# Performance work log

Hardware: AMD Instinct MI355X
Metric: run time of the kernel (lower is better)

The kernel has to match this reference:

```python
import jax, jax.numpy as jnp
import numpy as np

N, E, G, D, L, EA = 100000, 1600000, 128, 128, 3, 7
BN_EPS = 1e-5


def _bn(x, g, b, m, v):
    # eval-mode BatchNorm1d with running stats
    return (x - m) * (g / jnp.sqrt(v + BN_EPS)) + b


def setup_inputs() -> dict:
    key = jax.random.key(0)
    ks = iter(jax.random.split(key, 64))
    nrm = lambda shape, s: jax.random.normal(next(ks), shape, jnp.float32) * s
    unif = lambda shape: jax.random.uniform(next(ks), shape, jnp.float32) * 0.5 + 0.5
    inp = {
        # forward tensor args
        'x': jnp.zeros((N,), jnp.int32),  # indices into Embedding(1, D) -> all zero
        'edge_index': jax.random.randint(next(ks), (2, E), 0, N, jnp.int32),
        'edge_attr': nrm((E, EA), 1.0),
        'batch': jnp.sort(jax.random.randint(next(ks), (N,), 0, G, jnp.int32)),
        # embeddings
        'node_emb': nrm((1, D), 1.0),
        'vn_emb': nrm((1, D), 0.1),
        # per-layer GINConv params (stacked on leading layer dim)
        'edge_W': nrm((L, EA, D), EA ** -0.5), 'edge_b': jnp.zeros((L, D), jnp.float32),
        'eps': jnp.zeros((L,), jnp.float32),
        'mlp_W1': nrm((L, D, 2 * D), D ** -0.5), 'mlp_b1': jnp.zeros((L, 2 * D), jnp.float32),
        'mbn_g': jnp.ones((L, 2 * D), jnp.float32), 'mbn_b': jnp.zeros((L, 2 * D), jnp.float32),
        'mbn_m': nrm((L, 2 * D), 0.1), 'mbn_v': unif((L, 2 * D)),
        'mlp_W2': nrm((L, 2 * D, D), (2 * D) ** -0.5), 'mlp_b2': jnp.zeros((L, D), jnp.float32),
        # outer per-layer BatchNorm
        'bn_g': jnp.ones((L, D), jnp.float32), 'bn_b': jnp.zeros((L, D), jnp.float32),
        'bn_m': nrm((L, D), 0.1), 'bn_v': unif((L, D)),
        # virtual-node MLPs (L-1 of them)
        'vn_W1': nrm((L - 1, D, 2 * D), D ** -0.5), 'vn_b1': jnp.zeros((L - 1, 2 * D), jnp.float32),
        'vbn1_g': jnp.ones((L - 1, 2 * D), jnp.float32), 'vbn1_b': jnp.zeros((L - 1, 2 * D), jnp.float32),
        'vbn1_m': nrm((L - 1, 2 * D), 0.1), 'vbn1_v': unif((L - 1, 2 * D)),
        'vn_W2': nrm((L - 1, 2 * D, D), (2 * D) ** -0.5), 'vn_b2': jnp.zeros((L - 1, D), jnp.float32),
        'vbn2_g': jnp.ones((L - 1, D), jnp.float32), 'vbn2_b': jnp.zeros((L - 1, D), jnp.float32),
        'vbn2_m': nrm((L - 1, D), 0.1), 'vbn2_v': unif((L - 1, D)),
    }
    return inp


def reference(x, edge_index, edge_attr, batch, node_emb, vn_emb,
              edge_W, edge_b, eps, mlp_W1, mlp_b1, mbn_g, mbn_b, mbn_m, mbn_v,
              mlp_W2, mlp_b2, bn_g, bn_b, bn_m, bn_v,
              vn_W1, vn_b1, vbn1_g, vbn1_b, vbn1_m, vbn1_v,
              vn_W2, vn_b2, vbn2_g, vbn2_b, vbn2_m, vbn2_v):
    src, dst = edge_index[0], edge_index[1]
    h = node_emb[x]                                # [N, D] node encoder gather
    vn = jnp.broadcast_to(vn_emb[0], (G, D))       # virtual node per graph
    for l in range(L):
        h_in = h + vn[batch]                       # broadcast virtual node to nodes
        # GINConv
        e = edge_attr @ edge_W[l] + edge_b[l]      # [E, D]
        msg = jax.nn.relu(h_in[src] + e)           # gather + edge fuse
        agg = jax.ops.segment_sum(msg, dst, num_segments=N)
        z = (1.0 + eps[l]) * h_in + agg
        z = jax.nn.relu(_bn(z @ mlp_W1[l] + mlp_b1[l], mbn_g[l], mbn_b[l], mbn_m[l], mbn_v[l]))
        h2 = z @ mlp_W2[l] + mlp_b2[l]
        # outer BatchNorm (+ relu except last layer; dropout is identity in eval)
        h2 = _bn(h2, bn_g[l], bn_b[l], bn_m[l], bn_v[l])
        h = h2 if l == L - 1 else jax.nn.relu(h2)
        if l < L - 1:
            vt = jax.ops.segment_sum(h_in, batch, num_segments=G) + vn  # global_add_pool
            t = jax.nn.relu(_bn(vt @ vn_W1[l] + vn_b1[l], vbn1_g[l], vbn1_b[l], vbn1_m[l], vbn1_v[l]))
            vn = jax.nn.relu(_bn(t @ vn_W2[l] + vn_b2[l], vbn2_g[l], vbn2_b[l], vbn2_m[l], vbn2_v[l]))
    return h  # JK == 'last'
```

## Files before the change

kernel.cpp:

```cpp
#include <hip/hip_runtime.h>
#include <hip/hip_bf16.h>

#define NN 100000
#define NP 100032
#define EE 1600000
#define GG 128
#define DD 128
#define LL 3
#define EAA 7
#define BN_EPS 1e-5f

typedef __attribute__((ext_vector_type(8))) short bf16x8;
typedef __attribute__((ext_vector_type(4))) float f32x4;
typedef __attribute__((ext_vector_type(4))) unsigned short u16x4;
typedef _Float16 f16x2 __attribute__((ext_vector_type(2)));

__device__ __forceinline__ unsigned short f2bf(float x) {
    unsigned int u = __float_as_uint(x);
    u = (u + 0x7FFF + ((u >> 16) & 1)) >> 16;
    return (unsigned short)u;
}
__device__ __forceinline__ float bf2f(unsigned short h) {
    return __uint_as_float(((unsigned int)h) << 16);
}
__device__ __forceinline__ float bflo(unsigned int u) {
    return __uint_as_float(u << 16);
}
__device__ __forceinline__ float bfhi(unsigned int u) {
    return __uint_as_float(u & 0xFFFF0000u);
}
__device__ __forceinline__ unsigned int pkf16(float a, float b) {
    f16x2 v = {(_Float16)a, (_Float16)b};
    return __builtin_bit_cast(unsigned int, v);
}

#if __has_builtin(__builtin_amdgcn_fdot2)
#define DOT2(q, w, c) __builtin_amdgcn_fdot2((q), (w), (c), false)
#else
__device__ __forceinline__ float dot2_sw(f16x2 a, f16x2 b, float c) {
    return fmaf((float)a.x, (float)b.x, fmaf((float)a.y, (float)b.y, c));
}
#define DOT2(q, w, c) dot2_sw((q), (w), (c))
#endif

__global__ __launch_bounds__(256) void init_kernel(
    const int* __restrict__ x, const float* __restrict__ node_emb,
    const float* __restrict__ vn_emb, float* __restrict__ h,
    float* __restrict__ vn)
{
    long i = (long)blockIdx.x * 256 + threadIdx.x;
    if (i < (long)NN * DD) {
        int node = (int)(i >> 7), d = (int)(i & 127);
        h[i] = node_emb[(long)x[node] * DD + d];
    }
    if (i < GG * DD) vn[i] = vn_emb[i & 127];
}

#define R1 8
__global__ __launch_bounds__(256) void hin_kernel(
    float* __restrict__ hbuf,
    unsigned short* __restrict__ h16,
    const float* __restrict__ vn,
    const int* __restrict__ batch,
    const float* __restrict__ eps,
    float* __restrict__ agg,
    float* __restrict__ vt,
    int layer, int accum_vt, int write_agg)
{
    const int d  = threadIdx.x & 127;
    const int rg = threadIdx.x >> 7;
    const float epl = 1.0f + eps[layer];
    const long row0 = (long)blockIdx.x * (R1 * 2);

    float vacc = 0.0f;
    int   vb   = -1;
    #pragma unroll
    for (int r = 0; r < R1; ++r) {
        long row = row0 + rg + 2 * r;
        if (row >= NN) break;
        int b = batch[row];
        long idx = row * DD + d;
        float hv = hbuf[idx] + vn[(long)b * DD + d];
        hbuf[idx] = hv;
        h16[idx]  = f2bf(hv);
        if (write_agg) agg[idx] = epl * hv;
        if (accum_vt) {
            if (b != vb) {
                if (vb >= 0) atomicAdd(&vt[(long)vb * DD + d], vacc);
                vb = b; vacc = 0.0f;
            }
            vacc += hv;
        }
    }
    if (accum_vt && vb >= 0) atomicAdd(&vt[(long)vb * DD + d], vacc);
}

__global__ __launch_bounds__(256) void vt_kernel(
    const float* __restrict__ hbuf, const int* __restrict__ batch,
    float* __restrict__ vt)
{
    const int d  = threadIdx.x & 127;
    const int rg = threadIdx.x >> 7;
    const long row0 = (long)blockIdx.x * 16;
    float vacc = 0.0f;
    int   vb   = -1;
    #pragma unroll
    for (int r = 0; r < 8; ++r) {
        long row = row0 + rg + 2 * r;
        if (row >= NN) break;
        int b = batch[row];
        float hv = hbuf[row * DD + d];
        if (b != vb) {
            if (vb >= 0) atomicAdd(&vt[(long)vb * DD + d], vacc);
            vb = b; vacc = 0.0f;
        }
        vacc += hv;
    }
    if (vb >= 0) atomicAdd(&vt[(long)vb * DD + d], vacc);
}

__global__ __launch_bounds__(256) void cnt_kernel(
    const int* __restrict__ batch, int* __restrict__ cnt)
{
    const int tid = blockIdx.x * 256 + threadIdx.x;
    const int CH  = (NN + 16383) / 16384;
    long s = (long)tid * CH;
    long e = s + CH; if (e > NN) e = NN;
    int vb = -1, c = 0;
    for (long i = s; i < e; ++i) {
        int b = batch[i];
        if (b != vb) { if (vb >= 0) atomicAdd(&cnt[vb], c); vb = b; c = 0; }
        ++c;
    }
    if (vb >= 0) atomicAdd(&cnt[vb], c);
}

__global__ __launch_bounds__(256) void count_kernel(
    const int* __restrict__ ei, int* __restrict__ deg)
{
    long e = (long)blockIdx.x * 256 + threadIdx.x;
    if (e < EE) atomicAdd(&deg[ei[EE + e]], 1);
}

__global__ __launch_bounds__(1024) void scan_a(
    const int* __restrict__ deg, int* __restrict__ rp, int* __restrict__ partials)
{
    __shared__ int s[1024];
    int t = threadIdx.x;
    long i = (long)blockIdx.x * 1024 + t;
    int v = (i < NN) ? deg[i] : 0;
    s[t] = v;
    __syncthreads();
    for (int off = 1; off < 1024; off <<= 1) {
        int u = (t >= off) ? s[t - off] : 0;
        __syncthreads();
        s[t] += u;
        __syncthreads();
    }
    if (i < NN) rp[i] = s[t] - v;
    if (t == 1023) partials[blockIdx.x] = s[1023];
}

__global__ void scan_b(int* __restrict__ partials, int nb)
{
    if (threadIdx.x == 0) {
        int run = 0;
        for (int i = 0; i < nb; ++i) { int v = partials[i]; partials[i] = run; run += v; }
    }
}

__global__ __launch_bounds__(1024) void scan_c(
    int* __restrict__ rp, int* __restrict__ fill, const int* __restrict__ partials)
{
    long i = (long)blockIdx.x * 1024 + threadIdx.x;
    if (i < NN) {
        int v = rp[i] + partials[blockIdx.x];
        rp[i] = v;
        fill[i] = v;
    }
    if (i == 0) rp[NN] = EE;
}

__global__ __launch_bounds__(256) void scatter_kernel(
    const int* __restrict__ ei, const float* __restrict__ eattr,
    int* __restrict__ fill, unsigned int* __restrict__ attr16,
    int* __restrict__ src_arr, int* __restrict__ eid_perm)
{
    long e = (long)blockIdx.x * 256 + threadIdx.x;
    if (e >= EE) return;
    int dst = ei[EE + e];
    int pos = atomicAdd(&fill[dst], 1);
    if (attr16) {
        uint4 w;
        w.x = pkf16(eattr[e * EAA + 0], eattr[e * EAA + 1]);
        w.y = pkf16(eattr[e * EAA + 2], eattr[e * EAA + 3]);
        w.z = pkf16(eattr[e * EAA + 4], eattr[e * EAA + 5]);
        w.w = pkf16(eattr[e * EAA + 6], 0.0f);
        *(uint4*)(attr16 + (long)pos * 4) = w;
        src_arr[pos] = ei[e];
    } else {
        eid_perm[pos] = (int)e;
    }
}

#define WPAIR_PREAMBLE(eWl)                                                   \
    f16x2 wx[4], wy[4];                                                       \
    {                                                                         \
        _Pragma("unroll")                                                     \
        for (int j = 0; j < 3; ++j) {                                         \
            float2 p0 = *(const float2*)&(eWl)[(2 * j) * DD + d0];            \
            float2 p1 = *(const float2*)&(eWl)[(2 * j + 1) * DD + d0];        \
            wx[j] = (f16x2){(_Float16)p0.x, (_Float16)p1.x};                  \
            wy[j] = (f16x2){(_Float16)p0.y, (_Float16)p1.y};                  \
        }                                                                     \
        float2 p6 = *(const float2*)&(eWl)[6 * DD + d0];                      \
        wx[3] = (f16x2){(_Float16)p6.x, (_Float16)0.0f};                      \
        wy[3] = (f16x2){(_Float16)p6.y, (_Float16)0.0f};                      \
    }

#define EDOT(AU, EX, EY)                                                      \
    float EX = bias.x, EY = bias.y;                                           \
    {                                                                         \
        f16x2 q0 = __builtin_bit_cast(f16x2, AU.x);                           \
        f16x2 q1 = __builtin_bit_cast(f16x2, AU.y);                           \
        f16x2 q2 = __builtin_bit_cast(f16x2, AU.z);                           \
        f16x2 q3 = __builtin_bit_cast(f16x2, AU.w);                           \
        EX = DOT2(q0, wx[0], EX); EY = DOT2(q0, wy[0], EY);                   \
        EX = DOT2(q1, wx[1], EX); EY = DOT2(q1, wy[1], EY);                   \
        EX = DOT2(q2, wx[2], EX); EY = DOT2(q2, wy[2], EY);                   \
        EX = DOT2(q3, wx[3], EX); EY = DOT2(q3, wy[3], EY);                   \
    }

__global__ __launch_bounds__(256) void gin0_kernel(
    const float* __restrict__ node_emb,
    const float* __restrict__ vn_emb,
    const int* __restrict__ rp,
    const unsigned int* __restrict__ attr16,
    const float* __restrict__ eW, const float* __restrict__ eb,
    const float* __restrict__ eps,
    unsigned short* __restrict__ aggh, unsigned short* __restrict__ aggl)
{
    const int lane = threadIdx.x & 63;
    const int wid  = __builtin_amdgcn_readfirstlane(threadIdx.x >> 6);
    const int n    = blockIdx.x * 4 + wid;
    const int d0   = lane * 2;

    WPAIR_PREAMBLE(eW)
    const float2 bias = *(const float2*)&eb[d0];
    const float  epl  = 1.0f + eps[0];

    const float cx = node_emb[d0]     + vn_emb[d0];
    const float cy = node_emb[d0 + 1] + vn_emb[d0 + 1];
    float accx = epl * cx, accy = epl * cy;

    int p        = __builtin_amdgcn_readfirstlane(rp[n]);
    const int p1 = __builtin_amdgcn_readfirstlane(rp[n + 1]);

    #define EDGE0(AU)                                                         \
    {                                                                         \
        EDOT(AU, ex, ey)                                                      \
        float mx = cx + ex, my = cy + ey;                                     \
        accx += fmaxf(mx, 0.0f); accy += fmaxf(my, 0.0f);                     \
    }

    for (; p + 4 <= p1; p += 4) {
        const uint4* a4p = (const uint4*)(attr16 + (long)p * 4);
        uint4 A0 = a4p[0];
        uint4 A1 = a4p[1];
        uint4 A2 = a4p[2];
        uint4 A3 = a4p[3];
        EDGE0(A0)
        EDGE0(A1)
        EDGE0(A2)
        EDGE0(A3)
    }
    for (; p < p1; ++p) {
        uint4 A = *(const uint4*)(attr16 + (long)p * 4);
        EDGE0(A)
    }
    #undef EDGE0

    unsigned short hx = f2bf(accx), hy = f2bf(accy);
    *(unsigned int*)&aggh[(long)n * DD + d0] = (unsigned int)hx | ((unsigned int)hy << 16);
    *(unsigned int*)&aggl[(long)n * DD + d0] =
        (unsigned int)f2bf(accx - bf2f(hx)) | ((unsigned int)f2bf(accy - bf2f(hy)) << 16);
}

__global__ __launch_bounds__(256) void gin_agg_kernel(
    const float* __restrict__ h_in,
    const unsigned short* __restrict__ h16,
    const int* __restrict__ rp,
    const unsigned int* __restrict__ attr16,
    const int* __restrict__ src_arr,
    const float* __restrict__ eW, const float* __restrict__ eb,
    const float* __restrict__ eps,
    unsigned short* __restrict__ aggh, unsigned short* __restrict__ aggl,
    int layer)
{
    const int lane = threadIdx.x & 63;
    const int wid  = __builtin_amdgcn_readfirstlane(threadIdx.x >> 6);
    const int n    = blockIdx.x * 4 + wid;
    const int d0   = lane * 2;

    const float* eWl = eW + (long)layer * EAA * DD;
    WPAIR_PREAMBLE(eWl)
    const float2 bias = *(const float2*)&eb[layer * DD + d0];
    const float  epl  = 1.0f + eps[layer];

    float2 hn = *(const float2*)&h_in[(long)n * DD + d0];
    float accx = epl * hn.x, accy = epl * hn.y;

    int p        = __builtin_amdgcn_readfirstlane(rp[n]);
    const int p1 = __builtin_amdgcn_readfirstlane(rp[n + 1]);

    #define EDGE(AU, GU)                                                      \
    {                                                                         \
        EDOT(AU, ex, ey)                                                      \
        float mx = bflo(GU) + ex, my = bfhi(GU) + ey;                         \
        accx += fmaxf(mx, 0.0f); accy += fmaxf(my, 0.0f);                     \
    }

    for (; p + 4 <= p1; p += 4) {
        int4 sv = *(const int4*)(src_arr + p);
        int s0 = __builtin_amdgcn_readfirstlane(sv.x);
        int s1 = __builtin_amdgcn_readfirstlane(sv.y);
        int s2 = __builtin_amdgcn_readfirstlane(sv.z);
        int s3 = __builtin_amdgcn_readfirstlane(sv.w);
        const uint4* a4p = (const uint4*)(attr16 + (long)p * 4);
        uint4 A0 = a4p[0];
        uint4 A1 = a4p[1];
        uint4 A2 = a4p[2];
        uint4 A3 = a4p[3];
        unsigned int g0 = *(const unsigned int*)(h16 + (long)s0 * DD + d0);
        unsigned int g1 = *(const unsigned int*)(h16 + (long)s1 * DD + d0);
        unsigned int g2 = *(const unsigned int*)(h16 + (long)s2 * DD + d0);
        unsigned int g3 = *(const unsigned int*)(h16 + (long)s3 * DD + d0);
        EDGE(A0, g0)
        EDGE(A1, g1)
        EDGE(A2, g2)
        EDGE(A3, g3)
    }
    for (; p < p1; ++p) {
        int s = __builtin_amdgcn_readfirstlane(src_arr[p]);
        uint4 A = *(const uint4*)(attr16 + (long)p * 4);
        unsigned int g = *(const unsigned int*)(h16 + (long)s * DD + d0);
        EDGE(A, g)
    }
    #undef EDGE

    unsigned short hx = f2bf(accx), hy = f2bf(accy);
    *(unsigned int*)&aggh[(long)n * DD + d0] = (unsigned int)hx | ((unsigned int)hy << 16);
    *(unsigned int*)&aggl[(long)n * DD + d0] =
        (unsigned int)f2bf(accx - bf2f(hx)) | ((unsigned int)f2bf(accy - bf2f(hy)) << 16);
}

__global__ __launch_bounds__(256) void gin_agg_eid_kernel(
    const float* __restrict__ h_in,
    const int* __restrict__ rp,
    const int* __restrict__ eid_perm,
    const int* __restrict__ ei,
    const float* __restrict__ eattr,
    const float* __restrict__ eW, const float* __restrict__ eb,
    const float* __restrict__ eps,
    float* __restrict__ agg, int layer)
{
    const int d    = threadIdx.x & 127;
    const int half = threadIdx.x >> 7;
    const long n   = (long)blockIdx.x * 2 + half;

    float w[EAA];
    #pragma unroll
    for (int a = 0; a < EAA; ++a) w[a] = eW[layer * EAA * DD + a * DD + d];
    const float bias = eb[layer * DD + d];
    const float epl  = 1.0f + eps[layer];

    float acc = epl * h_in[n * DD + d];
    const int p0 = rp[n], p1 = rp[n + 1];
    for (int p = p0; p < p1; ++p) {
        int e = eid_perm[p];
        int src = ei[e];
        float ea = bias;
        #pragma unroll
        for (int a = 0; a < EAA; ++a)
            ea = fmaf(eattr[(long)e * EAA + a], w[a], ea);
        float m = h_in[(long)src * DD + d] + ea;
        acc += m > 0.0f ? m : 0.0f;
    }
    agg[n * DD + d] = acc;
}

#define EPB 64
__global__ __launch_bounds__(256) void edge_kernel(
    const float* __restrict__ h_in,
    const int* __restrict__ ei,
    const float* __restrict__ eattr,
    const float* __restrict__ eW,
    const float* __restrict__ eb,
    float* __restrict__ agg,
    int layer)
{
    const int d    = threadIdx.x & 127;
    const int esub = threadIdx.x >> 7;
    float w[EAA];
    #pragma unroll
    for (int a = 0; a < EAA; ++a) w[a] = eW[layer * EAA * DD + a * DD + d];
    const float bias = eb[layer * DD + d];

    const long base = (long)blockIdx.x * EPB;
    for (int k = esub; k < EPB; k += 2) {
        long e = base + k;
        if (e >= EE) break;
        int s = ei[e];
        int t = ei[EE + e];
        float acc = bias;
        #pragma unroll
        for (int a = 0; a < EAA; ++a)
            acc = fmaf(eattr[e * EAA + a], w[a], acc);
        float m = h_in[(long)s * DD + d] + acc;
        m = m > 0.0f ? m : 0.0f;
        atomicAdd(&agg[(long)t * DD + d], m);
    }
}

__global__ __launch_bounds__(256) void wprep_kernel(
    const float* __restrict__ W1, const float* __restrict__ W2,
    unsigned short* __restrict__ w1h, unsigned short* __restrict__ w1l,
    unsigned short* __restrict__ w2h, unsigned short* __restrict__ w2l)
{
    int tid = blockIdx.x * 256 + threadIdx.x;
    if (tid >= LL * 2 * 32768) return;
    int l = tid / 65536;
    int rem = tid - l * 65536;
    int mat = rem >> 15;
    int fi = rem & 32767;
    int b = fi & 7, lane = (fi >> 3) & 63;
    int kgrp = ((lane >> 4) << 3) + b;
    if (mat == 0) {
        int mt = (fi >> 9) & 15, kk = fi >> 13;
        int m = (mt << 4) + (lane & 15);
        int k = (kk << 5) + kgrp;
        float v = W1[(long)l * DD * 2 * DD + (long)k * 2 * DD + m];
        unsigned short hi = f2bf(v);
        w1h[(long)l * 32768 + fi] = hi;
        w1l[(long)l * 32768 + fi] = f2bf(v - bf2f(hi));
    } else {
        int mt = (fi >> 9) & 7, kk = fi >> 12;
        int m = (mt << 4) + (lane & 15);
        int k = (kk << 5) + kgrp;
        float v = W2[(long)l * 2 * DD * DD + (long)k * DD + m];
        unsigned short hi = f2bf(v);
        w2h[(long)l * 32768 + fi] = hi;
        w2l[(long)l * 32768 + fi] = f2bf(v - bf2f(hi));
    }
}

__global__ __launch_bounds__(256) void bnprep_kernel(
    const float* __restrict__ b1, const float* __restrict__ g1,
    const float* __restrict__ be1, const float* __restrict__ m1,
    const float* __restrict__ v1,
    const float* __restrict__ b2, const float* __restrict__ g2,
    const float* __restrict__ be2, const float* __restrict__ m2,
    const float* __restrict__ v2,
    float* __restrict__ sc1, float* __restrict__ sh1,
    float* __restrict__ sc2, float* __restrict__ sh2)
{
    int tid = blockIdx.x * 256 + threadIdx.x;
    if (tid < LL * 2 * DD) {
        float sc = g1[tid] / sqrtf(v1[tid] + BN_EPS);
        sc1[tid] = sc;
        sh1[tid] = (b1[tid] - m1[tid]) * sc + be1[tid];
    }
    int t2 = tid - LL * 2 * DD;
    if (t2 >= 0 && t2 < LL * DD) {
        float sc = g2[t2] / sqrtf(v2[t2] + BN_EPS);
        sc2[t2] = sc;
        sh2[t2] = (b2[t2] - m2[t2]) * sc + be2[t2];
    }
}

__global__ __launch_bounds__(256, 2) void mlp_mfma_kernel(
    const float* __restrict__ z_in,
    const unsigned short* __restrict__ z16h, const unsigned short* __restrict__ z16l,
    int zfmt,
    const unsigned short* __restrict__ w1h, const unsigned short* __restrict__ w1l,
    const unsigned short* __restrict__ w2h, const unsigned short* __restrict__ w2l,
    const float* __restrict__ sc1, const float* __restrict__ sh1,
    const float* __restrict__ sc2, const float* __restrict__ sh2,
    float* __restrict__ h_out, int layer, int do_relu,
    const int* __restrict__ batch, const float* __restrict__ vnbuf,
    unsigned short* __restrict__ h16, int fuse)
{
    __shared__ char lds[65536];
    const int tid  = threadIdx.x;
    const int lane = tid & 63;
    const int wv   = tid >> 6;
    const long row0 = (long)blockIdx.x * 64;
    const int kb = (lane >> 4) << 3;

    if (zfmt) {
        const uint4* zh = (const uint4*)(z16h + row0 * DD);
        const uint4* zl = (const uint4*)(z16l + row0 * DD);
        #pragma unroll
        for (int i = 0; i < 4; ++i) {
            int idx = tid + i * 256;
            uint4 hv = zh[idx];
            uint4 lv = zl[idx];
            int r = idx >> 4;
            int c = (idx & 15) << 3;
            int off = ((r << 8) + (c << 1)) ^ ((r & 7) << 4);
            *(uint4*)(lds + off)         = hv;
            *(uint4*)(lds + 16384 + off) = lv;
        }
    } else {
        const float4* zi = (const float4*)(z_in + row0 * DD);
        #pragma unroll
        for (int i = 0; i < 8; ++i) {
            int idx = tid + i * 256;
            float4 v = zi[idx];
            int r = idx >> 5;
            int c = (idx & 31) << 2;
            u16x4 hv, lv;
            hv.x = f2bf(v.x); lv.x = f2bf(v.x - bf2f(hv.x));
            hv.y = f2bf(v.y); lv.y = f2bf(v.y - bf2f(hv.y));
            hv.z = f2bf(v.z); lv.z = f2bf(v.z - bf2f(hv.z));
            hv.w = f2bf(v.w); lv.w = f2bf(v.w - bf2f(hv.w));
            int off = ((r << 8) + (c << 1)) ^ ((r & 7) << 4);
            *(u16x4*)(lds + off)         = hv;
            *(u16x4*)(lds + 16384 + off) = lv;
        }
    }
    __syncthreads();

    bf16x8 B1h[4][4], B1l[4][4];
    #pragma unroll
    for (int nt = 0; nt < 4; ++nt) {
        int r = (nt << 4) + (lane & 15);
        #pragma unroll
        for (int kk = 0; kk < 4; ++kk) {
            int off = ((r << 8) + (((kk << 5) + kb) << 1)) ^ ((r & 7) << 4);
            B1h[nt][kk] = *(const bf16x8*)(lds + off);
            B1l[nt][kk] = *(const bf16x8*)(lds + 16384 + off);
        }
    }
    __syncthreads();

    const unsigned short* w1hl = w1h + (long)layer * 32768;
    const unsigned short* w1ll = w1l + (long)layer * 32768;
    #pragma unroll
    for (int mtl = 0; mtl < 4; ++mtl) {
        const int mt = (wv << 2) + mtl;
        bf16x8 Ah[4], Al[4];
        #pragma unroll
        for (int kk = 0; kk < 4; ++kk) {
            const long boff = ((long)((kk << 4) + mt) * 64 + lane) << 3;
            Ah[kk] = *(const bf16x8*)(w1hl + boff);
            Al[kk] = *(const bf16x8*)(w1ll + boff);
        }
        f32x4 acc[4];
        #pragma unroll
        for (int nt = 0; nt < 4; ++nt) acc[nt] = (f32x4){0.f, 0.f, 0.f, 0.f};
        #pragma unroll
        for (int kk = 0; kk < 4; ++kk) {
            #pragma unroll
            for (int nt = 0; nt < 4; ++nt) {
                acc[nt] = __builtin_amdgcn_mfma_f32_16x16x32_bf16(Ah[kk], B1h[nt][kk], acc[nt], 0, 0, 0);
                acc[nt] = __builtin_amdgcn_mfma_f32_16x16x32_bf16(Ah[kk], B1l[nt][kk], acc[nt], 0, 0, 0);
                acc[nt] = __builtin_amdgcn_mfma_f32_16x16x32_bf16(Al[kk], B1h[nt][kk], acc[nt], 0, 0, 0);
            }
        }
        const int m0 = (mt << 4) + ((lane >> 4) << 2);
        const float4 s4 = *(const float4*)&sc1[layer * 2 * DD + m0];
        const float4 t4 = *(const float4*)&sh1[layer * 2 * DD + m0];
        #pragma unroll
        for (int nt = 0; nt < 4; ++nt) {
            int row = (nt << 4) + (lane & 15);
            float u0 = fmaxf(fmaf(acc[nt][0], s4.x, t4.x), 0.0f);
            float u1 = fmaxf(fmaf(acc[nt][1], s4.y, t4.y), 0.0f);
            float u2 = fmaxf(fmaf(acc[nt][2], s4.z, t4.z), 0.0f);
            float u3 = fmaxf(fmaf(acc[nt][3], s4.w, t4.w), 0.0f);
            u16x4 hv, lv;
            hv.x = f2bf(u0); lv.x = f2bf(u0 - bf2f(hv.x));
            hv.y = f2bf(u1); lv.y = f2bf(u1 - bf2f(hv.y));
            hv.z = f2bf(u2); lv.z = f2bf(u2 - bf2f(hv.z));
            hv.w = f2bf(u3); lv.w = f2bf(u3 - bf2f(hv.w));
            int off = ((row << 9) + (m0 << 1)) ^ ((row & 7) << 4);
            *(u16x4*)(lds + off)         = hv;
            *(u16x4*)(lds + 32768 + off) = lv;
        }
    }
    __syncthreads();

    const unsigned short* w2hl = w2h + (long)layer * 32768;
    const unsigned short* w2ll = w2l + (long)layer * 32768;
    f32x4 acc2[2][4];
    #pragma unroll
    for (int mtl = 0; mtl < 2; ++mtl)
        #pragma unroll
        for (int nt = 0; nt < 4; ++nt) acc2[mtl][nt] = (f32x4){0.f, 0.f, 0.f, 0.f};

    #pragma unroll
    for (int kk = 0; kk < 8; ++kk) {
        bf16x8 Bh[4], Bl[4];
        #pragma unroll
        for (int nt = 0; nt < 4; ++nt) {
            int r = (nt << 4) + (lane & 15);
            int off = ((r << 9) + (((kk << 5) + kb) << 1)) ^ ((r & 7) << 4);
            Bh[nt] = *(const bf16x8*)(lds + off);
            Bl[nt] = *(const bf16x8*)(lds + 32768 + off);
        }
        #pragma unroll
        for (int mtl = 0; mtl < 2; ++mtl) {
            const int mt = (wv << 1) + mtl;
            const long boff = ((long)((kk << 3) + mt) * 64 + lane) << 3;
            bf16x8 Ah = *(const bf16x8*)(w2hl + boff);
            bf16x8 Al = *(const bf16x8*)(w2ll + boff);
            #pragma unroll
            for (int nt = 0; nt < 4; ++nt) {
                acc2[mtl][nt] = __builtin_amdgcn_mfma_f32_16x16x32_bf16(Ah, Bh[nt], acc2[mtl][nt], 0, 0, 0);
                acc2[mtl][nt] = __builtin_amdgcn_mfma_f32_16x16x32_bf16(Ah, Bl[nt], acc2[mtl][nt], 0, 0, 0);
                acc2[mtl][nt] = __builtin_amdgcn_mfma_f32_16x16x32_bf16(Al, Bh[nt], acc2[mtl][nt], 0, 0, 0);
            }
        }
    }
    #pragma unroll
    for (int mtl = 0; mtl < 2; ++mtl) {
        const int m0 = ((((wv << 1) + mtl)) << 4) + ((lane >> 4) << 2);
        const float4 s4 = *(const float4*)&sc2[layer * DD + m0];
        const float4 t4 = *(const float4*)&sh2[layer * DD + m0];
        #pragma unroll
        for (int nt = 0; nt < 4; ++nt) {
            long row = row0 + (nt << 4) + (lane & 15);
            if (row < NN) {
                float o0 = fmaf(acc2[mtl][nt][0], s4.x, t4.x);
                float o1 = fmaf(acc2[mtl][nt][1], s4.y, t4.y);
                float o2 = fmaf(acc2[mtl][nt][2], s4.z, t4.z);
                float o3 = fmaf(acc2[mtl][nt][3], s4.w, t4.w);
                if (do_relu) {
                    o0 = fmaxf(o0, 0.0f); o1 = fmaxf(o1, 0.0f);
                    o2 = fmaxf(o2, 0.0f); o3 = fmaxf(o3, 0.0f);
                }
                if (fuse) {
                    int b = batch[row];
                    float4 vnv = *(const float4*)&vnbuf[(long)b * DD + m0];
                    o0 += vnv.x; o1 += vnv.y; o2 += vnv.z; o3 += vnv.w;
                    u16x4 hv;
                    hv.x = f2bf(o0); hv.y = f2bf(o1);
                    hv.z = f2bf(o2); hv.w = f2bf(o3);
                    *(u16x4*)&h16[row * DD + m0] = hv;
                }
                *(float4*)&h_out[row * DD + m0] = make_float4(o0, o1, o2, o3);
            }
        }
    }
}

__global__ __launch_bounds__(256) void vn_kernel(
    const float* __restrict__ vt, float* __restrict__ vn,
    const float* __restrict__ W1, const float* __restrict__ b1,
    const float* __restrict__ g1, const float* __restrict__ be1,
    const float* __restrict__ m1, const float* __restrict__ v1,
    const float* __restrict__ W2, const float* __restrict__ b2,
    const float* __restrict__ g2, const float* __restrict__ be2,
    const float* __restrict__ m2, const float* __restrict__ v2,
    int layer)
{
    __shared__ float row[DD];
    __shared__ float u[2 * DD];
    const int g = blockIdx.x;
    const int t = threadIdx.x;

    if (t < DD) row[t] = vt[(long)g * DD + t] + vn[(long)g * DD + t];
    __syncthreads();

    {
        const float* W = W1 + (long)layer * DD * 2 * DD;
        float acc = 0.0f;
        for (int k = 0; k < DD; ++k) acc = fmaf(row[k], W[k * 2 * DD + t], acc);
        const long o = (long)layer * 2 * DD + t;
        float sc = g1[o] / sqrtf(v1[o] + BN_EPS);
        float sh = be1[o] - m1[o] * sc;
        float val = (acc + b1[o]) * sc + sh;
        u[t] = val > 0.0f ? val : 0.0f;
    }
    __syncthreads();

    if (t < DD) {
        const float* W = W2 + (long)layer * 2 * DD * DD;
        float acc = 0.0f;
        for (int k = 0; k < 2 * DD; ++k) acc = fmaf(u[k], W[k * DD + t], acc);
        const long o = (long)layer * DD + t;
        float sc = g2[o] / sqrtf(v2[o] + BN_EPS);
        float sh = be2[o] - m2[o] * sc;
        float val = (acc + b2[o]) * sc + sh;
        vn[(long)g * DD + t] = val > 0.0f ? val : 0.0f;
    }
}

__global__ __launch_bounds__(256) void vn0_kernel(
    const int* __restrict__ cnt,
    const float* __restrict__ node_emb, const float* __restrict__ vn_emb,
    float* __restrict__ vn,
    const float* __restrict__ W1, const float* __restrict__ b1,
    const float* __restrict__ g1, const float* __restrict__ be1,
    const float* __restrict__ m1, const float* __restrict__ v1,
    const float* __restrict__ W2, const float* __restrict__ b2,
    const float* __restrict__ g2, const float* __restrict__ be2,
    const float* __restrict__ m2, const float* __restrict__ v2)
{
    __shared__ float row[DD];
    __shared__ float u[2 * DD];
    const int g = blockIdx.x;
    const int t = threadIdx.x;

    if (t < DD) {
        float c = node_emb[t] + vn_emb[t];
        row[t] = (float)cnt[g] * c + vn_emb[t];
    }
    __syncthreads();

    {
        float acc = 0.0f;
        for (int k = 0; k < DD; ++k) acc = fmaf(row[k], W1[k * 2 * DD + t], acc);
        float sc = g1[t] / sqrtf(v1[t] + BN_EPS);
        float sh = be1[t] - m1[t] * sc;
        float val = (acc + b1[t]) * sc + sh;
        u[t] = val > 0.0f ? val : 0.0f;
    }
    __syncthreads();

    if (t < DD) {
        float acc = 0.0f;
        for (int k = 0; k < 2 * DD; ++k) acc = fmaf(u[k], W2[k * DD + t], acc);
        float sc = g2[t] / sqrtf(v2[t] + BN_EPS);
        float sh = be2[t] - m2[t] * sc;
        float val = (acc + b2[t]) * sc + sh;
        vn[(long)g * DD + t] = val > 0.0f ? val : 0.0f;
    }
}

extern "C" void kernel_launch(void* const* d_in, const int* in_sizes, int n_in,
                              void* d_out, int out_size, void* d_ws, size_t ws_size,
                              hipStream_t stream)
{
    const int*   x       = (const int*)  d_in[0];
    const int*   ei      = (const int*)  d_in[1];
    const float* eattr   = (const float*)d_in[2];
    const int*   batch   = (const int*)  d_in[3];
    const float* node_emb= (const float*)d_in[4];
    const float* vn_emb  = (const float*)d_in[5];
    const float* edge_W  = (const float*)d_in[6];
    const float* edge_b  = (const float*)d_in[7];
    const float* eps     = (const float*)d_in[8];
    const float* mlp_W1  = (const float*)d_in[9];
    const float* mlp_b1  = (const float*)d_in[10];
    const float* mbn_g   = (const float*)d_in[11];
    const float* mbn_b   = (const float*)d_in[12];
    const float* mbn_m   = (const float*)d_in[13];
    const float* mbn_v   = (const float*)d_in[14];
    const float* mlp_W2  = (const float*)d_in[15];
    const float* mlp_b2  = (const float*)d_in[16];
    const float* bn_g    = (const float*)d_in[17];
    const float* bn_b    = (const float*)d_in[18];
    const float* bn_m    = (const float*)d_in[19];
    const float* bn_v    = (const float*)d_in[20];
    const float* vn_W1   = (const float*)d_in[21];
    const float* vn_b1   = (const float*)d_in[22];
    const float* vbn1_g  = (const float*)d_in[23];
    const float* vbn1_b  = (const float*)d_in[24];
    const float* vbn1_m  = (const float*)d_in[25];
    const float* vbn1_v  = (const float*)d_in[26];
    const float* vn_W2   = (const float*)d_in[27];
    const float* vn_b2   = (const float*)d_in[28];
    const float* vbn2_g  = (const float*)d_in[29];
    const float* vbn2_b  = (const float*)d_in[30];
    const float* vbn2_m  = (const float*)d_in[31];
    const float* vbn2_v  = (const float*)d_in[32];

    float* h = (float*)d_out;
    char*  ws = (char*)d_ws;

    size_t off = 0;
    auto alloc = [&](size_t bytes) -> void* {
        void* p = ws + off;
        off += (bytes + 255) & ~(size_t)255;
        return p;
    };
    const size_t GDB = (size_t)GG * DD * sizeof(float);

    float* agg      = (float*)alloc((size_t)NP * DD * sizeof(float));
    unsigned short* aggh = (unsigned short*)agg;
    unsigned short* aggl = aggh + (size_t)NP * DD;
    unsigned short* h16 = (unsigned short*)alloc((size_t)NN * DD * sizeof(unsigned short));
    float* vn       = (float*)alloc(GDB);
    float* vt       = (float*)alloc(GDB);
    int*   rp       = (int*)  alloc((NN + 1) * sizeof(int));
    int*   fill     = (int*)  alloc(NN * sizeof(int));
    int*   partials = (int*)  alloc(128 * sizeof(int));
    int*   cnt      = (int*)  alloc(GG * sizeof(int));
    int*   src_arr  = (int*)  alloc((size_t)EE * sizeof(int));
    unsigned short* w1h = (unsigned short*)alloc(LL * 32768 * sizeof(unsigned short));
    unsigned short* w1l = (unsigned short*)alloc(LL * 32768 * sizeof(unsigned short));
    unsigned short* w2h = (unsigned short*)alloc(LL * 32768 * sizeof(unsigned short));
    unsigned short* w2l = (unsigned short*)alloc(LL * 32768 * sizeof(unsigned short));
    float* bn1sc = (float*)alloc(LL * 2 * DD * sizeof(float));
    float* bn1sh = (float*)alloc(LL * 2 * DD * sizeof(float));
    float* bn2sc = (float*)alloc(LL * DD * sizeof(float));
    float* bn2sh = (float*)alloc(LL * DD * sizeof(float));
    const size_t base_end = off;

    unsigned int* attr16 = nullptr;
    int* eid_perm = nullptr;
    if (ws_size >= base_end + (size_t)EE * 4 * sizeof(unsigned int))
        attr16 = (unsigned int*)alloc((size_t)EE * 4 * sizeof(unsigned int));
    else if (ws_size >= base_end + (size_t)EE * sizeof(int))
        eid_perm = (int*)alloc((size_t)EE * sizeof(int));

    wprep_kernel<<<(LL * 2 * 32768 + 255) / 256, 256, 0, stream>>>(
        mlp_W1, mlp_W2, w1h, w1l, w2h, w2l);
    bnprep_kernel<<<(LL * 2 * DD + LL * DD + 255) / 256, 256, 0, stream>>>(
        mlp_b1, mbn_g, mbn_b, mbn_m, mbn_v,
        mlp_b2, bn_g, bn_b, bn_m, bn_v,
        bn1sc, bn1sh, bn2sc, bn2sh);

    const bool csr = (attr16 != nullptr) || (eid_perm != nullptr);
    if (csr) {
        const int egrid = (EE + 255) / 256;
        const int ngrid = (NN + 1023) / 1024;
        hipMemsetAsync(fill, 0, NN * sizeof(int), stream);
        count_kernel<<<egrid, 256, 0, stream>>>(ei, fill);
        scan_a<<<ngrid, 1024, 0, stream>>>(fill, rp, partials);
        scan_b<<<1, 64, 0, stream>>>(partials, ngrid);
        scan_c<<<ngrid, 1024, 0, stream>>>(rp, fill, partials);
        scatter_kernel<<<egrid, 256, 0, stream>>>(ei, eattr, fill, attr16, src_arr, eid_perm);
    }

    if (attr16) {
        hipMemsetAsync(cnt, 0, GG * sizeof(int), stream);
        cnt_kernel<<<64, 256, 0, stream>>>(batch, cnt);

        vn0_kernel<<<GG, 256, 0, stream>>>(
            cnt, node_emb, vn_emb, vn,
            vn_W1, vn_b1, vbn1_g, vbn1_b, vbn1_m, vbn1_v,
            vn_W2, vn_b2, vbn2_g, vbn2_b, vbn2_m, vbn2_v);
        gin0_kernel<<<NN / 4, 256, 0, stream>>>(
            node_emb, vn_emb, rp, attr16, edge_W, edge_b, eps, aggh, aggl);
        mlp_mfma_kernel<<<NP / 64, 256, 0, stream>>>(
            agg, aggh, aggl, 1, w1h, w1l, w2h, w2l, bn1sc, bn1sh, bn2sc, bn2sh,
            h, 0, 1, batch, vn, h16, 1);

        hipMemsetAsync(vt, 0, GDB, stream);
        vt_kernel<<<NN / 16, 256, 0, stream>>>(h, batch, vt);
        vn_kernel<<<GG, 256, 0, stream>>>(
            vt, vn, vn_W1, vn_b1, vbn1_g, vbn1_b, vbn1_m, vbn1_v,
            vn_W2, vn_b2, vbn2_g, vbn2_b, vbn2_m, vbn2_v, 1);
        gin_agg_kernel<<<NN / 4, 256, 0, stream>>>(
            h, h16, rp, attr16, src_arr, edge_W, edge_b, eps, aggh, aggl, 1);
        mlp_mfma_kernel<<<NP / 64, 256, 0, stream>>>(
            agg, aggh, aggl, 1, w1h, w1l, w2h, w2l, bn1sc, bn1sh, bn2sc, bn2sh,
            h, 1, 1, batch, vn, h16, 1);

        gin_agg_kernel<<<NN / 4, 256, 0, stream>>>(
            h, h16, rp, attr16, src_arr, edge_W, edge_b, eps, aggh, aggl, 2);
        mlp_mfma_kernel<<<NP / 64, 256, 0, stream>>>(
            agg, aggh, aggl, 1, w1h, w1l, w2h, w2l, bn1sc, bn1sh, bn2sc, bn2sh,
            h, 2, 0, batch, vn, h16, 0);
    } else {
        {
            long total = (long)NN * DD;
            init_kernel<<<(int)((total + 255) / 256), 256, 0, stream>>>(
                x, node_emb, vn_emb, h, vn);
        }
        for (int l = 0; l < LL; ++l) {
            int accum = (l < LL - 1) ? 1 : 0;
            if (accum)
                hipMemsetAsync(vt, 0, GDB, stream);

            hin_kernel<<<NN / (R1 * 2), 256, 0, stream>>>(
                h, h16, vn, batch, eps, agg, vt, l, accum, 1);

            if (eid_perm) {
                gin_agg_eid_kernel<<<NN / 2, 256, 0, stream>>>(
                    h, rp, eid_perm, ei, eattr, edge_W, edge_b, eps, agg, l);
            } else {
                edge_kernel<<<(EE + EPB - 1) / EPB, 256, 0, stream>>>(
                    h, ei, eattr, edge_W, edge_b, agg, l);
            }

            mlp_mfma_kernel<<<NP / 64, 256, 0, stream>>>(
                agg, nullptr, nullptr, 0, w1h, w1l, w2h, w2l,
                bn1sc, bn1sh, bn2sc, bn2sh,
                h, l, accum, batch, vn, h16, 0);

            if (accum)
                vn_kernel<<<GG, 256, 0, stream>>>(
                    vt, vn, vn_W1, vn_b1, vbn1_g, vbn1_b, vbn1_m, vbn1_v,
                    vn_W2, vn_b2, vbn2_g, vbn2_b, vbn2_m, vbn2_v, l);
        }
    }
}
```

Baseline: 653.3 us.

## Split CSR scatter into permutation pass and coalesced gather; prefetch next edge batch

The edge scatter is split in two. The first pass only does the atomic slot assignment and writes an edge-id permutation. The second pass runs in CSR order, reading edge attributes by permuted id and writing packed attr16 and src_arr with coalesced stores instead of scattered ones. Separately, the GIN aggregation loop software-pipelines the src-index and attribute loads for the next group of four edges while the current group is computed. This costs an extra kernel launch and an extra edge-sized buffer, plus more registers in the aggregation kernel.

```diff
diff --git a/kernel.cpp b/kernel.cpp
--- a/kernel.cpp
+++ b/kernel.cpp
@@ -181,26 +181,32 @@
     if (i == 0) rp[NN] = EE;
 }
 
-__global__ __launch_bounds__(256) void scatter_kernel(
-    const int* __restrict__ ei, const float* __restrict__ eattr,
-    int* __restrict__ fill, unsigned int* __restrict__ attr16,
-    int* __restrict__ src_arr, int* __restrict__ eid_perm)
+__global__ __launch_bounds__(256) void scatter_a_kernel(
+    const int* __restrict__ ei, int* __restrict__ fill,
+    int* __restrict__ eid_perm)
 {
     long e = (long)blockIdx.x * 256 + threadIdx.x;
     if (e >= EE) return;
     int dst = ei[EE + e];
     int pos = atomicAdd(&fill[dst], 1);
-    if (attr16) {
-        uint4 w;
-        w.x = pkf16(eattr[e * EAA + 0], eattr[e * EAA + 1]);
-        w.y = pkf16(eattr[e * EAA + 2], eattr[e * EAA + 3]);
-        w.z = pkf16(eattr[e * EAA + 4], eattr[e * EAA + 5]);
-        w.w = pkf16(eattr[e * EAA + 6], 0.0f);
-        *(uint4*)(attr16 + (long)pos * 4) = w;
-        src_arr[pos] = ei[e];
-    } else {
-        eid_perm[pos] = (int)e;
-    }
+    eid_perm[pos] = (int)e;
+}
+
+__global__ __launch_bounds__(256) void scatter_b_kernel(
+    const int* __restrict__ eid_perm,
+    const int* __restrict__ ei, const float* __restrict__ eattr,
+    unsigned int* __restrict__ attr16, int* __restrict__ src_arr)
+{
+    long p = (long)blockIdx.x * 256 + threadIdx.x;
+    if (p >= EE) return;
+    long e = eid_perm[p];
+    uint4 w;
+    w.x = pkf16(eattr[e * EAA + 0], eattr[e * EAA + 1]);
+    w.y = pkf16(eattr[e * EAA + 2], eattr[e * EAA + 3]);
+    w.z = pkf16(eattr[e * EAA + 4], eattr[e * EAA + 5]);
+    w.w = pkf16(eattr[e * EAA + 6], 0.0f);
+    *(uint4*)(attr16 + p * 4) = w;
+    src_arr[p] = ei[e];
 }
 
 #define WPAIR_PREAMBLE(eWl)                                                   \
@@ -320,25 +326,41 @@
         accx += fmaxf(mx, 0.0f); accy += fmaxf(my, 0.0f);                     \
     }
 
-    for (; p + 4 <= p1; p += 4) {
+    #define GATHER4(SV, G0, G1, G2, G3)                                       \
+        int s0_##G0 = __builtin_amdgcn_readfirstlane(SV.x);                   \
+        int s1_##G0 = __builtin_amdgcn_readfirstlane(SV.y);                   \
+        int s2_##G0 = __builtin_amdgcn_readfirstlane(SV.z);                   \
+        int s3_##G0 = __builtin_amdgcn_readfirstlane(SV.w);                   \
+        unsigned int G0 = *(const unsigned int*)(h16 + (long)s0_##G0 * DD + d0); \
+        unsigned int G1 = *(const unsigned int*)(h16 + (long)s1_##G0 * DD + d0); \
+        unsigned int G2 = *(const unsigned int*)(h16 + (long)s2_##G0 * DD + d0); \
+        unsigned int G3 = *(const unsigned int*)(h16 + (long)s3_##G0 * DD + d0);
+
+    if (p + 4 <= p1) {
         int4 sv = *(const int4*)(src_arr + p);
-        int s0 = __builtin_amdgcn_readfirstlane(sv.x);
-        int s1 = __builtin_amdgcn_readfirstlane(sv.y);
-        int s2 = __builtin_amdgcn_readfirstlane(sv.z);
-        int s3 = __builtin_amdgcn_readfirstlane(sv.w);
         const uint4* a4p = (const uint4*)(attr16 + (long)p * 4);
-        uint4 A0 = a4p[0];
-        uint4 A1 = a4p[1];
-        uint4 A2 = a4p[2];
-        uint4 A3 = a4p[3];
-        unsigned int g0 = *(const unsigned int*)(h16 + (long)s0 * DD + d0);
-        unsigned int g1 = *(const unsigned int*)(h16 + (long)s1 * DD + d0);
-        unsigned int g2 = *(const unsigned int*)(h16 + (long)s2 * DD + d0);
-        unsigned int g3 = *(const unsigned int*)(h16 + (long)s3 * DD + d0);
-        EDGE(A0, g0)
-        EDGE(A1, g1)
-        EDGE(A2, g2)
-        EDGE(A3, g3)
+        uint4 A0 = a4p[0], A1 = a4p[1], A2 = a4p[2], A3 = a4p[3];
+
+        while (p + 8 <= p1) {
+            GATHER4(sv, g0, g1, g2, g3)
+            int4 svn = *(const int4*)(src_arr + p + 4);
+            const uint4* b4p = (const uint4*)(attr16 + (long)(p + 4) * 4);
+            uint4 B0 = b4p[0], B1 = b4p[1], B2 = b4p[2], B3 = b4p[3];
+            EDGE(A0, g0)
+            EDGE(A1, g1)
+            EDGE(A2, g2)
+            EDGE(A3, g3)
+            sv = svn; A0 = B0; A1 = B1; A2 = B2; A3 = B3;
+            p += 4;
+        }
+        {
+            GATHER4(sv, g0, g1, g2, g3)
+            EDGE(A0, g0)
+            EDGE(A1, g1)
+            EDGE(A2, g2)
+            EDGE(A3, g3)
+            p += 4;
+        }
     }
     for (; p < p1; ++p) {
         int s = __builtin_amdgcn_readfirstlane(src_arr[p]);
@@ -346,6 +368,7 @@
         unsigned int g = *(const unsigned int*)(h16 + (long)s * DD + d0);
         EDGE(A, g)
     }
+    #undef GATHER4
     #undef EDGE
 
     unsigned short hx = f2bf(accx), hy = f2bf(accy);
@@ -798,6 +821,7 @@
     int*   partials = (int*)  alloc(128 * sizeof(int));
     int*   cnt      = (int*)  alloc(GG * sizeof(int));
     int*   src_arr  = (int*)  alloc((size_t)EE * sizeof(int));
+    int*   eid_perm = (int*)  alloc((size_t)EE * sizeof(int));
     unsigned short* w1h = (unsigned short*)alloc(LL * 32768 * sizeof(unsigned short));
     unsigned short* w1l = (unsigned short*)alloc(LL * 32768 * sizeof(unsigned short));
     unsigned short* w2h = (unsigned short*)alloc(LL * 32768 * sizeof(unsigned short));
@@ -809,11 +833,8 @@
     const size_t base_end = off;
 
     unsigned int* attr16 = nullptr;
-    int* eid_perm = nullptr;
     if (ws_size >= base_end + (size_t)EE * 4 * sizeof(unsigned int))
         attr16 = (unsigned int*)alloc((size_t)EE * 4 * sizeof(unsigned int));
-    else if (ws_size >= base_end + (size_t)EE * sizeof(int))
-        eid_perm = (int*)alloc((size_t)EE * sizeof(int));
 
     wprep_kernel<<<(LL * 2 * 32768 + 255) / 256, 256, 0, stream>>>(
         mlp_W1, mlp_W2, w1h, w1l, w2h, w2l);
@@ -822,8 +843,7 @@
         mlp_b2, bn_g, bn_b, bn_m, bn_v,
         bn1sc, bn1sh, bn2sc, bn2sh);
 
-    const bool csr = (attr16 != nullptr) || (eid_perm != nullptr);
-    if (csr) {
+    {
         const int egrid = (EE + 255) / 256;
         const int ngrid = (NN + 1023) / 1024;
         hipMemsetAsync(fill, 0, NN * sizeof(int), stream);
@@ -831,7 +851,10 @@
         scan_a<<<ngrid, 1024, 0, stream>>>(fill, rp, partials);
         scan_b<<<1, 64, 0, stream>>>(partials, ngrid);
         scan_c<<<ngrid, 1024, 0, stream>>>(rp, fill, partials);
-        scatter_kernel<<<egrid, 256, 0, stream>>>(ei, eattr, fill, attr16, src_arr, eid_perm);
+        scatter_a_kernel<<<egrid, 256, 0, stream>>>(ei, fill, eid_perm);
+        if (attr16)
+            scatter_b_kernel<<<egrid, 256, 0, stream>>>(
+                eid_perm, ei, eattr, attr16, src_arr);
     }
 
     if (attr16) {
@@ -878,13 +901,8 @@
             hin_kernel<<<NN / (R1 * 2), 256, 0, stream>>>(
                 h, h16, vn, batch, eps, agg, vt, l, accum, 1);
 
-            if (eid_perm) {
-                gin_agg_eid_kernel<<<NN / 2, 256, 0, stream>>>(
-                    h, rp, eid_perm, ei, eattr, edge_W, edge_b, eps, agg, l);
-            } else {
-                edge_kernel<<<(EE + EPB - 1) / EPB, 256, 0, stream>>>(
-                    h, ei, eattr, edge_W, edge_b, agg, l);
-            }
+            gin_agg_eid_kernel<<<NN / 2, 256, 0, stream>>>(
+                h, rp, eid_perm, ei, eattr, edge_W, edge_b, eps, agg, l);
 
             mlp_mfma_kernel<<<NP / 64, 256, 0, stream>>>(
                 agg, nullptr, nullptr, 0, w1h, w1l, w2h, w2l,
```

Measured after the change: 737.7 us. +12.9%, slower.
